# Optimization experiments

Hardware: AMD Instinct MI355X
Metric: run time of the kernel (lower is better)

## Reference

```python
import jax, jax.numpy as jnp
import numpy as np

H = 4      # heads
D = 32     # per-head / input channel dim
B, N = 1, 256


def setup_inputs() -> dict:
    key = jax.random.key(0)
    ks = jax.random.split(key, 10)
    x = jax.random.normal(ks[0], (B, N, N, D), dtype=jnp.float32)
    # binary key mask (1 = keep, 0 = masked out)
    mask = (jax.random.uniform(ks[1], (B, N, N)) > 0.15).astype(jnp.float32)
    s = 1.0 / np.sqrt(D)
    Wq = jax.random.normal(ks[2], (H * D, D), dtype=jnp.float32) * s
    bq = jnp.zeros((H * D,), dtype=jnp.float32)
    Wk = jax.random.normal(ks[3], (H * D, D), dtype=jnp.float32) * s
    bk = jnp.zeros((H * D,), dtype=jnp.float32)
    Wv = jax.random.normal(ks[4], (H * D, D), dtype=jnp.float32) * s
    bv = jnp.zeros((H * D,), dtype=jnp.float32)
    Wb = jax.random.normal(ks[5], (H, D), dtype=jnp.float32) * s
    bb = jnp.zeros((H,), dtype=jnp.float32)
    return {"x": x, "mask": mask, "Wq": Wq, "bq": bq, "Wk": Wk, "bk": bk,
            "Wv": Wv, "bv": bv, "Wb": Wb, "bb": bb}


def reference(x, mask, Wq, bq, Wk, bk, Wv, bv, Wb, bb):
    b_, i_, j_, d_ = x.shape
    # QKV projections -> [B, I, J, H, D]
    q = (x @ Wq.T + bq).reshape(b_, i_, j_, H, d_)
    k = (x @ Wk.T + bk).reshape(b_, i_, j_, H, d_)
    v = (x @ Wv.T + bv).reshape(b_, i_, j_, H, d_)
    # pairwise triangle bias: [B, I, J, H] -> [B, H, J, K]
    tri_b = jnp.transpose(x @ Wb.T + bb, (0, 3, 1, 2))
    scale = 1.0 / jnp.sqrt(jnp.asarray(d_, x.dtype))
    # scores over the key index k along the row: [B, H, I, J, K]
    scores = jnp.einsum('bijhd,bikhd->bhijk', q, k) * scale
    scores = scores + tri_b[:, :, None, :, :]                 # triangle bias
    scores = scores + (mask - 1.0)[:, None, :, None, :] * 1e9  # key mask
    attn = jax.nn.softmax(scores, axis=-1)
    out = jnp.einsum('bhijk,bikhd->bijhd', attn, v)  # [B, I, J, H, D]
    return out
```

## Files before the change

### kernel.cpp

```cpp
#include <hip/hip_runtime.h>

#define HEADS 4
#define NN 256
#define DW 32

typedef __bf16 bf16x8 __attribute__((ext_vector_type(8)));
typedef float f32x4 __attribute__((ext_vector_type(4)));
typedef float f32x16 __attribute__((ext_vector_type(16)));
typedef unsigned int u32x4 __attribute__((ext_vector_type(4)));
typedef unsigned short ushort4v __attribute__((ext_vector_type(4)));

static __device__ __forceinline__ ushort f2bf(float f) {
  __bf16 h = (__bf16)f;
  ushort r;
  __builtin_memcpy(&r, &h, 2);
  return r;
}

static __device__ __forceinline__ unsigned cvt_pk_bf16(float lo, float hi) {
  unsigned r;
  asm("v_cvt_pk_bf16_f32 %0, %1, %2" : "=v"(r) : "v"(lo), "v"(hi));
  return r;
}

__global__ __launch_bounds__(256) void bias_kernel(
    const float* __restrict__ x, const float* __restrict__ Wb,
    const float* __restrict__ bb, float* __restrict__ bias_t) {
  const int j = blockIdx.x;
  const int k = threadIdx.x;
  const float* xr = x + (j * NN + k) * DW;
  float xv[DW];
#pragma unroll
  for (int c = 0; c < 8; ++c) {
    const float4 v = reinterpret_cast<const float4*>(xr)[c];
    xv[c * 4 + 0] = v.x; xv[c * 4 + 1] = v.y;
    xv[c * 4 + 2] = v.z; xv[c * 4 + 3] = v.w;
  }
#pragma unroll
  for (int h = 0; h < HEADS; ++h) {
    float a0 = 0.f, a1 = 0.f;
#pragma unroll
    for (int d = 0; d < DW; d += 2) {
      a0 += xv[d] * Wb[h * DW + d];
      a1 += xv[d + 1] * Wb[h * DW + d + 1];
    }
    bias_t[(h * NN + k) * NN + j] = a0 + a1 + bb[h];
  }
}

__global__ __launch_bounds__(256, 3) void attn_mfma(
    const float* __restrict__ x, const float* __restrict__ mask,
    const float* __restrict__ Wq, const float* __restrict__ bq,
    const float* __restrict__ Wk, const float* __restrict__ bk,
    const float* __restrict__ Wv, const float* __restrict__ bv,
    const float* __restrict__ bias_t, float* __restrict__ out) {
  __shared__ ushort Kq[NN][40];
  __shared__ ushort Vt[DW][264];
  __shared__ float mk[NN];
  __shared__ float Ls[NN];

  const int bid = blockIdx.x;
  const int i = bid >> 2;
  const int h = bid & 3;
  const int t = threadIdx.x;
  const int w = t >> 6;
  const int l = t & 63;
  const int lo5 = l & 31;
  const int hi = l >> 5;
  const int lr = l & 15;
  const int lq = l >> 4;
  const int rowbase = w * 64;
  const float scale = 0.17677669529663687f;

  bf16x8 wqf[2], wkf[2], wvf[2];
#pragma unroll
  for (int nt = 0; nt < 2; ++nt) {
    const int dd = nt * 16 + lr;
    const float* rq = Wq + (h * DW + dd) * DW + lq * 8;
    const float* rk = Wk + (h * DW + dd) * DW + lq * 8;
    const float* rv = Wv + (h * DW + dd) * DW + lq * 8;
#pragma unroll
    for (int jj = 0; jj < 8; ++jj) {
      wqf[nt][jj] = (__bf16)rq[jj];
      wkf[nt][jj] = (__bf16)rk[jj];
      wvf[nt][jj] = (__bf16)rv[jj];
    }
  }

  bf16x8 af[4];
#pragma unroll
  for (int rt = 0; rt < 4; ++rt) {
    const float* xr = x + (i * NN + rowbase + rt * 16 + lr) * DW + lq * 8;
#pragma unroll
    for (int jj = 0; jj < 8; ++jj) af[rt][jj] = (__bf16)xr[jj];
  }

#pragma unroll
  for (int rt = 0; rt < 4; ++rt) {
#pragma unroll
    for (int nt = 0; nt < 2; ++nt) {
      const int dd = nt * 16 + lr;
      f32x4 z = {0.f, 0.f, 0.f, 0.f};
      f32x4 cq = __builtin_amdgcn_mfma_f32_16x16x32_bf16(af[rt], wqf[nt], z, 0, 0, 0);
      const float bqv = bq[h * DW + dd];
#pragma unroll
      for (int j = 0; j < 4; ++j)
        Kq[rowbase + rt * 16 + lq * 4 + j][dd] = f2bf((cq[j] + bqv) * scale);
    }
  }
  bf16x8 qb[2][2];
#pragma unroll
  for (int qt = 0; qt < 2; ++qt)
#pragma unroll
    for (int dh = 0; dh < 2; ++dh)
      qb[qt][dh] = *(const bf16x8*)&Kq[rowbase + qt * 32 + lo5][dh * 16 + 8 * hi];
  __syncthreads();

#pragma unroll
  for (int rt = 0; rt < 4; ++rt) {
#pragma unroll
    for (int nt = 0; nt < 2; ++nt) {
      const int dd = nt * 16 + lr;
      f32x4 z = {0.f, 0.f, 0.f, 0.f};
      f32x4 ck = __builtin_amdgcn_mfma_f32_16x16x32_bf16(af[rt], wkf[nt], z, 0, 0, 0);
      f32x4 cv = __builtin_amdgcn_mfma_f32_16x16x32_bf16(af[rt], wvf[nt], z, 0, 0, 0);
      const float bkv = bk[h * DW + dd];
      const float bvv = bv[h * DW + dd];
#pragma unroll
      for (int j = 0; j < 4; ++j)
        Kq[rowbase + rt * 16 + lq * 4 + j][dd] = f2bf(ck[j] + bkv);
      ushort4v v4;
#pragma unroll
      for (int j = 0; j < 4; ++j) v4[j] = f2bf(cv[j] + bvv);
      *(ushort4v*)&Vt[dd][rowbase + rt * 16 + lq * 4] = v4;
    }
  }
  mk[t] = mask[i * NN + t];
  __syncthreads();

  f32x16 ot[2];
  float lsum[2] = {0.f, 0.f};
#pragma unroll
  for (int qt = 0; qt < 2; ++qt)
#pragma unroll
    for (int r = 0; r < 16; ++r) ot[qt][r] = 0.f;

  const float* bbase = bias_t + (h * NN) * NN;

  for (int kb = 0; kb < 8; ++kb) {
    const int kbase = kb * 32;
    float mv[16];
#pragma unroll
    for (int r = 0; r < 16; ++r)
      mv[r] = mk[kbase + (r & 3) + 8 * (r >> 2) + 4 * hi];

    const bf16x8 ka0 = *(const bf16x8*)&Kq[kbase + lo5][8 * hi];
    const bf16x8 ka1 = *(const bf16x8*)&Kq[kbase + lo5][16 + 8 * hi];
    const bf16x8 va0 = *(const bf16x8*)&Vt[lo5][kbase + 8 * hi];
    const bf16x8 va1 = *(const bf16x8*)&Vt[lo5][kbase + 16 + 8 * hi];

#pragma unroll
    for (int qt = 0; qt < 2; ++qt) {
      const int qrow = rowbase + qt * 32 + lo5;
      float bi[16];
      const float* bp = bbase + (kbase + 4 * hi) * NN + qrow;
#pragma unroll
      for (int r = 0; r < 16; ++r)
        bi[r] = bp[((r & 3) + 8 * (r >> 2)) * NN];

      f32x16 st;
      {
        f32x16 z;
#pragma unroll
        for (int r = 0; r < 16; ++r) z[r] = 0.f;
        st = __builtin_amdgcn_mfma_f32_32x32x16_bf16(ka0, qb[qt][0], z, 0, 0, 0);
        st = __builtin_amdgcn_mfma_f32_32x32x16_bf16(ka1, qb[qt][1], st, 0, 0, 0);
      }

      float pm[16];
      float ls = 0.f;
#pragma unroll
      for (int r = 0; r < 16; ++r) {
        const float p = __expf(st[r] + bi[r]) * mv[r];
        pm[r] = p;
        ls += p;
      }
      lsum[qt] += ls;

#pragma unroll
      for (int half = 0; half < 2; ++half) {
        const int b0 = half * 8;
        unsigned w0, w1, w2, w3;
        {
          unsigned A = cvt_pk_bf16(pm[b0 + 0], pm[b0 + 1]);
          unsigned B = cvt_pk_bf16(pm[b0 + 4], pm[b0 + 5]);
          asm volatile("v_permlane32_swap_b32 %0, %1" : "+v"(A), "+v"(B));
          w0 = A; w2 = B;
        }
        {
          unsigned A = cvt_pk_bf16(pm[b0 + 2], pm[b0 + 3]);
          unsigned B = cvt_pk_bf16(pm[b0 + 6], pm[b0 + 7]);
          asm volatile("v_permlane32_swap_b32 %0, %1" : "+v"(A), "+v"(B));
          w1 = A; w3 = B;
        }
        u32x4 words = {w0, w1, w2, w3};
        const bf16x8 pf = __builtin_bit_cast(bf16x8, words);
        ot[qt] = __builtin_amdgcn_mfma_f32_32x32x16_bf16(
            pf, half ? va1 : va0, ot[qt], 0, 0, 0);
      }
    }
  }

#pragma unroll
  for (int qt = 0; qt < 2; ++qt) {
    const float ls = lsum[qt] + __shfl_xor(lsum[qt], 32);
    Ls[rowbase + qt * 32 + lo5] = 1.0f / ls;
  }

#pragma unroll
  for (int qt = 0; qt < 2; ++qt)
#pragma unroll
    for (int r = 0; r < 16; ++r) {
      const int qp = (r & 3) + 8 * (r >> 2) + 4 * hi;
      const int qrow = rowbase + qt * 32 + qp;
      out[((i * NN + qrow) * HEADS + h) * DW + lo5] = ot[qt][r] * Ls[qrow];
    }
}

extern "C" void kernel_launch(void* const* d_in, const int* in_sizes, int n_in,
                              void* d_out, int out_size, void* d_ws,
                              size_t ws_size, hipStream_t stream) {
  const float* x    = (const float*)d_in[0];
  const float* mask = (const float*)d_in[1];
  const float* Wq   = (const float*)d_in[2];
  const float* bq   = (const float*)d_in[3];
  const float* Wk   = (const float*)d_in[4];
  const float* bk   = (const float*)d_in[5];
  const float* Wv   = (const float*)d_in[6];
  const float* bv   = (const float*)d_in[7];
  const float* Wb   = (const float*)d_in[8];
  const float* bb   = (const float*)d_in[9];
  float* out = (float*)d_out;
  float* bias_t = (float*)d_ws;

  bias_kernel<<<NN, 256, 0, stream>>>(x, Wb, bb, bias_t);
  attn_mfma<<<NN * HEADS, 256, 0, stream>>>(x, mask, Wq, bq, Wk, bk, Wv, bv,
                                            bias_t, out);
}
```

Before: 118.4 us.

## Restructure bias kernel, use exp2 softmax, raise occupancy and prioritize MFMA

Result: slower. 158.9 us (+34.2%).

```diff
diff --git a/kernel.cpp b/kernel.cpp
--- a/kernel.cpp
+++ b/kernel.cpp
@@ -3,6 +3,7 @@
 #define HEADS 4
 #define NN 256
 #define DW 32
+#define LOG2E 1.4426950408889634f
 
 typedef __bf16 bf16x8 __attribute__((ext_vector_type(8)));
 typedef float f32x4 __attribute__((ext_vector_type(4)));
@@ -26,38 +27,41 @@
 __global__ __launch_bounds__(256) void bias_kernel(
     const float* __restrict__ x, const float* __restrict__ Wb,
     const float* __restrict__ bb, float* __restrict__ bias_t) {
-  const int j = blockIdx.x;
+  const int jt = blockIdx.x;
+  const int h = blockIdx.y;
   const int k = threadIdx.x;
-  const float* xr = x + (j * NN + k) * DW;
-  float xv[DW];
-#pragma unroll
-  for (int c = 0; c < 8; ++c) {
-    const float4 v = reinterpret_cast<const float4*>(xr)[c];
-    xv[c * 4 + 0] = v.x; xv[c * 4 + 1] = v.y;
-    xv[c * 4 + 2] = v.z; xv[c * 4 + 3] = v.w;
-  }
-#pragma unroll
-  for (int h = 0; h < HEADS; ++h) {
+  float wb[DW];
+#pragma unroll
+  for (int d = 0; d < DW; ++d) wb[d] = Wb[h * DW + d];
+  const float bbv = bb[h];
+  float b[8];
+#pragma unroll
+  for (int jj = 0; jj < 8; ++jj) {
+    const float* xr = x + ((jt * 8 + jj) * NN + k) * DW;
     float a0 = 0.f, a1 = 0.f;
 #pragma unroll
-    for (int d = 0; d < DW; d += 2) {
-      a0 += xv[d] * Wb[h * DW + d];
-      a1 += xv[d + 1] * Wb[h * DW + d + 1];
-    }
-    bias_t[(h * NN + k) * NN + j] = a0 + a1 + bb[h];
-  }
-}
-
-__global__ __launch_bounds__(256, 3) void attn_mfma(
+    for (int c = 0; c < 8; ++c) {
+      const float4 v = reinterpret_cast<const float4*>(xr)[c];
+      a0 += v.x * wb[c * 4 + 0] + v.z * wb[c * 4 + 2];
+      a1 += v.y * wb[c * 4 + 1] + v.w * wb[c * 4 + 3];
+    }
+    b[jj] = (a0 + a1 + bbv) * LOG2E;
+  }
+  float* dst = bias_t + (h * NN + k) * NN + jt * 8;
+  *reinterpret_cast<float4*>(dst) = make_float4(b[0], b[1], b[2], b[3]);
+  *reinterpret_cast<float4*>(dst + 4) = make_float4(b[4], b[5], b[6], b[7]);
+}
+
+__global__ __launch_bounds__(256, 4) void attn_mfma(
     const float* __restrict__ x, const float* __restrict__ mask,
     const float* __restrict__ Wq, const float* __restrict__ bq,
     const float* __restrict__ Wk, const float* __restrict__ bk,
     const float* __restrict__ Wv, const float* __restrict__ bv,
     const float* __restrict__ bias_t, float* __restrict__ out) {
-  __shared__ ushort Kq[NN][40];
-  __shared__ ushort Vt[DW][264];
-  __shared__ float mk[NN];
-  __shared__ float Ls[NN];
+  __shared__ __align__(16) ushort Kq[NN][40];
+  __shared__ __align__(16) ushort Vt[DW][264];
+  __shared__ __align__(16) float mk[NN];
+  __shared__ __align__(16) float Ls[NN];
 
   const int bid = blockIdx.x;
   const int i = bid >> 2;
@@ -70,7 +74,7 @@
   const int lr = l & 15;
   const int lq = l >> 4;
   const int rowbase = w * 64;
-  const float scale = 0.17677669529663687f;
+  const float scale = 0.17677669529663687f * LOG2E;
 
   bf16x8 wqf[2], wkf[2], wvf[2];
 #pragma unroll
@@ -114,7 +118,6 @@
 #pragma unroll
     for (int dh = 0; dh < 2; ++dh)
       qb[qt][dh] = *(const bf16x8*)&Kq[rowbase + qt * 32 + lo5][dh * 16 + 8 * hi];
-  __syncthreads();
 
 #pragma unroll
   for (int rt = 0; rt < 4; ++rt) {
@@ -147,12 +150,13 @@
 
   const float* bbase = bias_t + (h * NN) * NN;
 
+#pragma unroll 1
   for (int kb = 0; kb < 8; ++kb) {
     const int kbase = kb * 32;
-    float mv[16];
-#pragma unroll
-    for (int r = 0; r < 16; ++r)
-      mv[r] = mk[kbase + (r & 3) + 8 * (r >> 2) + 4 * hi];
+    float4 mvv[4];
+#pragma unroll
+    for (int g = 0; g < 4; ++g)
+      mvv[g] = *(const float4*)&mk[kbase + 4 * hi + 8 * g];
 
     const bf16x8 ka0 = *(const bf16x8*)&Kq[kbase + lo5][8 * hi];
     const bf16x8 ka1 = *(const bf16x8*)&Kq[kbase + lo5][16 + 8 * hi];
@@ -173,16 +177,18 @@
         f32x16 z;
 #pragma unroll
         for (int r = 0; r < 16; ++r) z[r] = 0.f;
+        __builtin_amdgcn_s_setprio(1);
         st = __builtin_amdgcn_mfma_f32_32x32x16_bf16(ka0, qb[qt][0], z, 0, 0, 0);
         st = __builtin_amdgcn_mfma_f32_32x32x16_bf16(ka1, qb[qt][1], st, 0, 0, 0);
+        __builtin_amdgcn_s_setprio(0);
       }
 
-      float pm[16];
       float ls = 0.f;
 #pragma unroll
       for (int r = 0; r < 16; ++r) {
-        const float p = __expf(st[r] + bi[r]) * mv[r];
-        pm[r] = p;
+        const float p =
+            __builtin_amdgcn_exp2f(st[r] + bi[r]) * (&mvv[r >> 2].x)[r & 3];
+        st[r] = p;
         ls += p;
       }
       lsum[qt] += ls;
@@ -192,21 +198,23 @@
         const int b0 = half * 8;
         unsigned w0, w1, w2, w3;
         {
-          unsigned A = cvt_pk_bf16(pm[b0 + 0], pm[b0 + 1]);
-          unsigned B = cvt_pk_bf16(pm[b0 + 4], pm[b0 + 5]);
+          unsigned A = cvt_pk_bf16(st[b0 + 0], st[b0 + 1]);
+          unsigned B = cvt_pk_bf16(st[b0 + 4], st[b0 + 5]);
           asm volatile("v_permlane32_swap_b32 %0, %1" : "+v"(A), "+v"(B));
           w0 = A; w2 = B;
         }
         {
-          unsigned A = cvt_pk_bf16(pm[b0 + 2], pm[b0 + 3]);
-          unsigned B = cvt_pk_bf16(pm[b0 + 6], pm[b0 + 7]);
+          unsigned A = cvt_pk_bf16(st[b0 + 2], st[b0 + 3]);
+          unsigned B = cvt_pk_bf16(st[b0 + 6], st[b0 + 7]);
           asm volatile("v_permlane32_swap_b32 %0, %1" : "+v"(A), "+v"(B));
           w1 = A; w3 = B;
         }
         u32x4 words = {w0, w1, w2, w3};
         const bf16x8 pf = __builtin_bit_cast(bf16x8, words);
+        __builtin_amdgcn_s_setprio(1);
         ot[qt] = __builtin_amdgcn_mfma_f32_32x32x16_bf16(
             pf, half ? va1 : va0, ot[qt], 0, 0, 0);
+        __builtin_amdgcn_s_setprio(0);
       }
     }
   }
@@ -243,7 +251,7 @@
   float* out = (float*)d_out;
   float* bias_t = (float*)d_ws;
 
-  bias_kernel<<<NN, 256, 0, stream>>>(x, Wb, bb, bias_t);
+  bias_kernel<<<dim3(32, HEADS), 256, 0, stream>>>(x, Wb, bb, bias_t);
   attn_mfma<<<NN * HEADS, 256, 0, stream>>>(x, mask, Wq, bq, Wk, bk, Wv, bv,
                                             bias_t, out);
 }
```
